# Kernel tuning notes

Hardware: AMD Instinct MI355X
Metric: run time of the kernel (lower is better)

Reference implementation:

```python
import jax, jax.numpy as jnp
import numpy as np

B, LQ, LIM = 4, 640, 1296
D_MODEL, NHEAD, DFF, MAX_DIST = 768, 12, 3072, 100
DK = D_MODEL // NHEAD
EPS = 1e-5


def _layer_norm(x, g, b):
    mu = jnp.mean(x, axis=-1, keepdims=True)
    var = jnp.mean(jnp.square(x - mu), axis=-1, keepdims=True)
    return (x - mu) * jax.lax.rsqrt(var + EPS) * g + b


def setup_inputs() -> dict:
    key = jax.random.key(0)
    ks = jax.random.split(key, 24)
    s = 0.02
    inp = {
        "docqa": jax.random.normal(ks[0], (B, LQ, D_MODEL), jnp.float32),
        "im_tokens": jax.random.normal(ks[1], (B, LIM, D_MODEL), jnp.float32),
        "docqa_x": jax.random.randint(ks[2], (B, LQ), 0, 1000, jnp.int32),
        "docqa_y": jax.random.randint(ks[3], (B, LQ), 0, 1000, jnp.int32),
        "im_tokens_x": jax.random.randint(ks[4], (B, LIM), 0, 1000, jnp.int32),
        "im_tokens_y": jax.random.randint(ks[5], (B, LIM), 0, 1000, jnp.int32),
        # attention projection params
        "Wq": jax.random.normal(ks[6], (D_MODEL, D_MODEL), jnp.float32) * s,
        "bq": jnp.zeros((D_MODEL,), jnp.float32),
        "Wk": jax.random.normal(ks[7], (D_MODEL, D_MODEL), jnp.float32) * s,
        "bk": jnp.zeros((D_MODEL,), jnp.float32),
        "Wv": jax.random.normal(ks[8], (D_MODEL, D_MODEL), jnp.float32) * s,
        "bv": jnp.zeros((D_MODEL,), jnp.float32),
        "Wo": jax.random.normal(ks[9], (D_MODEL, D_MODEL), jnp.float32) * s,
        "bo": jnp.zeros((D_MODEL,), jnp.float32),
        # relative position bias tables: (2*max_dist+1, nhead) per axis
        "bias_x": jax.random.normal(ks[10], (2 * MAX_DIST + 1, NHEAD), jnp.float32) * s,
        "bias_y": jax.random.normal(ks[11], (2 * MAX_DIST + 1, NHEAD), jnp.float32) * s,
        # FFN
        "W1": jax.random.normal(ks[12], (D_MODEL, DFF), jnp.float32) * s,
        "b1": jnp.zeros((DFF,), jnp.float32),
        "W2": jax.random.normal(ks[13], (DFF, D_MODEL), jnp.float32) * s,
        "b2": jnp.zeros((D_MODEL,), jnp.float32),
        # LayerNorms
        "g1": jnp.ones((D_MODEL,), jnp.float32),
        "be1": jnp.zeros((D_MODEL,), jnp.float32),
        "g2": jnp.ones((D_MODEL,), jnp.float32),
        "be2": jnp.zeros((D_MODEL,), jnp.float32),
    }
    return inp


def reference(docqa, im_tokens, docqa_x, docqa_y, im_tokens_x, im_tokens_y,
              Wq, bq, Wk, bk, Wv, bv, Wo, bo, bias_x, bias_y,
              W1, b1, W2, b2, g1, be1, g2, be2):
    # keys/values attend over concatenated image tokens + docqa tokens
    full = jnp.concatenate([im_tokens, docqa], axis=1)            # (B, Lk, D)
    full_x = jnp.concatenate([im_tokens_x, docqa_x], axis=1)      # (B, Lk)
    full_y = jnp.concatenate([im_tokens_y, docqa_y], axis=1)

    q = (docqa @ Wq + bq).reshape(B, LQ, NHEAD, DK)               # (B,Lq,H,Dk)
    k = (full @ Wk + bk).reshape(B, LQ + LIM, NHEAD, DK)
    v = (full @ Wv + bv).reshape(B, LQ + LIM, NHEAD, DK)

    scores = jnp.einsum("bqhd,bkhd->bhqk", q, k) / jnp.sqrt(jnp.float32(DK))

    # relative-position bias, clamped to [-max_dist, max_dist]
    rel_x = jnp.clip(docqa_x[:, :, None] - full_x[:, None, :], -MAX_DIST, MAX_DIST) + MAX_DIST
    rel_y = jnp.clip(docqa_y[:, :, None] - full_y[:, None, :], -MAX_DIST, MAX_DIST) + MAX_DIST
    pos_bias = bias_x[rel_x] + bias_y[rel_y]                      # (B,Lq,Lk,H)
    scores = scores + jnp.transpose(pos_bias, (0, 3, 1, 2))       # (B,H,Lq,Lk)

    attn = jax.nn.softmax(scores, axis=-1)
    ctx = jnp.einsum("bhqk,bkhd->bqhd", attn, v).reshape(B, LQ, D_MODEL)
    attn_out = ctx @ Wo + bo

    # residual + norm + FFN + residual + norm (dropout=0 in eval)
    src = _layer_norm(docqa + attn_out, g1, be1)
    ffn = jnp.maximum(src @ W1 + b1, 0.0) @ W2 + b2
    src = _layer_norm(src + ffn, g2, be2)
    return src
```

## Files before the change

### kernel.cpp

```cpp
#include <hip/hip_runtime.h>
#include <hip/hip_bf16.h>

constexpr int B      = 4;
constexpr int LQ     = 640;
constexpr int LIM    = 1296;
constexpr int LK     = LQ + LIM;
constexpr int DM     = 768;
constexpr int NHEAD  = 12;
constexpr int DK     = 64;
constexpr int DFF    = 3072;
constexpr int MAXD   = 100;
constexpr int M_DOC  = B * LQ;
constexpr int M_FULL = B * LK;
constexpr size_t ML_CNT = (size_t)B * NHEAD * LQ;
constexpr int NPREP  = M_FULL * (DM / 8) / 256;
constexpr int NSPLIT = 3;

typedef __attribute__((ext_vector_type(8))) short bf16x8_t;
typedef __attribute__((ext_vector_type(4))) float f32x4_t;

__device__ __forceinline__ float b2f(__hip_bfloat16 x) { return __bfloat162float(x); }

__device__ __forceinline__ float ldf(const void* p, size_t i, int f32flag) {
    return f32flag ? ((const float*)p)[i]
                   : b2f(((const __hip_bfloat16*)p)[i]);
}

__device__ __forceinline__ void gl_lds16(const void* g, void* l) {
    __builtin_amdgcn_global_load_lds(
        (const __attribute__((address_space(1))) unsigned int*)g,
        (__attribute__((address_space(3))) unsigned int*)l, 16, 0, 0);
}

__device__ __forceinline__ void wtrans_tile(const void* W, __hip_bfloat16* Wt,
                                            int f32, int K, int N, int n0, int k0,
                                            __hip_bfloat16 (*t)[33])
{
    const int tx = threadIdx.x & 31, ty = threadIdx.x >> 5;
#pragma unroll
    for (int j = 0; j < 4; ++j) {
        int k = ty + j * 8;
        t[k][tx] = __float2bfloat16(ldf(W, (size_t)(k0 + k) * N + n0 + tx, f32));
    }
    __syncthreads();
#pragma unroll
    for (int j = 0; j < 4; ++j) {
        int n = ty + j * 8;
        Wt[(size_t)(n0 + n) * K + k0 + tx] = t[tx][n];
    }
}

__global__ __launch_bounds__(256)
void prep_wt3_kernel(const void* __restrict__ g1, int* __restrict__ flagp,
                     const void* __restrict__ im, const void* __restrict__ docqa,
                     const int* __restrict__ dqx, const int* __restrict__ dqy,
                     const int* __restrict__ imx, const int* __restrict__ imy,
                     const void* __restrict__ Wq, const void* __restrict__ Wk,
                     const void* __restrict__ Wv,
                     __hip_bfloat16* __restrict__ fullA,
                     int* __restrict__ cxy,
                     __hip_bfloat16* __restrict__ Wt3)
{
    __shared__ __hip_bfloat16 t[32][33];
    const bool f32 = ((*(const unsigned*)g1) & 0xFFFFu) == 0u;
    const int bx = blockIdx.x;

    if (bx >= NPREP) {
        const int id  = bx - NPREP;
        const int wid = id / 576;
        const int tt  = id % 576;
        const void* W = (wid == 0) ? Wq : (wid == 1) ? Wk : Wv;
        wtrans_tile(W, Wt3 + (size_t)wid * DM * DM, f32 ? 1 : 0, DM, DM,
                    (tt % 24) * 32, (tt / 24) * 32, t);
        return;
    }

    if (bx == 0 && threadIdx.x == 0) *flagp = f32 ? 1 : 0;

    const int gid = bx * 256 + threadIdx.x;
    if (gid < B * LK) {
        int b = gid / LK, l = gid - b * LK;
        const int x = (l < LIM) ? imx[b * LIM + l] : dqx[b * LQ + l - LIM];
        const int y = (l < LIM) ? imy[b * LIM + l] : dqy[b * LQ + l - LIM];
        cxy[gid] = (x & 0xFFFF) | (y << 16);
    }

    const int row = gid / (DM / 8);
    const int col = (gid - row * (DM / 8)) * 8;
    const int b   = row / LK;
    const int l   = row - b * LK;
    const size_t srow = (l < LIM) ? ((size_t)(b * LIM + l)) * DM
                                  : ((size_t)(b * LQ + (l - LIM))) * DM;
    const void* src = (l < LIM) ? im : docqa;
    union { bf16x8_t v; __hip_bfloat16 h[8]; } pk;
    if (f32) {
        const float4* fp = (const float4*)((const float*)src + srow + col);
        float4 a = fp[0], c = fp[1];
        pk.h[0] = __float2bfloat16(a.x); pk.h[1] = __float2bfloat16(a.y);
        pk.h[2] = __float2bfloat16(a.z); pk.h[3] = __float2bfloat16(a.w);
        pk.h[4] = __float2bfloat16(c.x); pk.h[5] = __float2bfloat16(c.y);
        pk.h[6] = __float2bfloat16(c.z); pk.h[7] = __float2bfloat16(c.w);
    } else {
        pk.v = *(const bf16x8_t*)((const __hip_bfloat16*)src + srow + col);
    }
    *(bf16x8_t*)(fullA + (size_t)row * DM + col) = pk.v;
}

__global__ __launch_bounds__(256)
void qkv_gemm(const __hip_bfloat16* __restrict__ fullA,
              const __hip_bfloat16* __restrict__ Wt3,
              const void* __restrict__ bq,
              const void* __restrict__ bk,
              const void* __restrict__ bv,
              __hip_bfloat16* __restrict__ qout,
              __hip_bfloat16* __restrict__ kb,
              __hip_bfloat16* __restrict__ vtb,
              const int* __restrict__ flagp)
{
    __shared__ __hip_bfloat16 Als[128 * 32];
    __shared__ __hip_bfloat16 Bls[128 * 32];

    const int f32  = *flagp;
    const int tid  = threadIdx.x;
    const int lane = tid & 63;
    const int wave = tid >> 6;
    const int quad = lane >> 4;
    const int c16  = lane & 15;

    const int id = blockIdx.x;
    int n0, m0;
    if (id < 732) {
        n0 = DM + (id % 12) * 128;
        m0 = (id / 12) * 128;
    } else {
        const int t = id - 732;
        n0 = (t % 6) * 128;
        m0 = (t / 6) * 128;
    }
    const int seg = n0 / DM;

    const int wm   = (wave >> 1) * 64;
    const int wn   = (wave & 1) * 64;
    constexpr int K = DM;

    f32x4_t acc[4][4] = {};

    for (int k0 = 0; k0 < K; k0 += 32) {
#pragma unroll
        for (int p = 0; p < 2; ++p) {
            const int lin = p * 64 + lane;
            int row = wave * 32 + (lin >> 2);
            int gr  = m0 + row;
            if (seg == 0) {
                const int bb = gr / LQ;
                gr = bb * LK + LIM + (gr - bb * LQ);
            } else if (gr > M_FULL - 1) gr = M_FULL - 1;
            gl_lds16(fullA + (size_t)gr * K + k0 + (lin & 3) * 8,
                     Als + wave * 1024 + p * 512);
        }
#pragma unroll
        for (int p = 0; p < 2; ++p) {
            const int lin = p * 64 + lane;
            const int row = wave * 32 + (lin >> 2);
            gl_lds16(Wt3 + (size_t)(n0 + row) * K + k0 + (lin & 3) * 8,
                     Bls + wave * 1024 + p * 512);
        }
        __syncthreads();

        bf16x8_t af[4], bfr[4];
#pragma unroll
        for (int i = 0; i < 4; ++i)
            af[i] = *(const bf16x8_t*)(Als + (wm + i * 16 + c16) * 32 + quad * 8);
#pragma unroll
        for (int j = 0; j < 4; ++j)
            bfr[j] = *(const bf16x8_t*)(Bls + (wn + j * 16 + c16) * 32 + quad * 8);
#pragma unroll
        for (int i = 0; i < 4; ++i)
#pragma unroll
            for (int j = 0; j < 4; ++j)
                acc[i][j] = __builtin_amdgcn_mfma_f32_16x16x32_bf16(af[i], bfr[j], acc[i][j], 0, 0, 0);
        __syncthreads();
    }

    const void* bptr = (seg == 0) ? bq : (seg == 1) ? bk : bv;
#pragma unroll
    for (int j = 0; j < 4; ++j) {
        const int col  = n0 + wn + j * 16 + c16;
        const int ncol = col - seg * DM;
        const float bj = ldf(bptr, ncol, f32);
        if (seg == 2) {
            const int h = ncol >> 6, d = ncol & 63;
#pragma unroll
            for (int i = 0; i < 4; ++i) {
                const int rowb = m0 + wm + i * 16 + quad * 4;
                const int bb0  = rowb / LK;
                const int l0   = rowb - bb0 * LK;
                if (l0 + 3 < LK && rowb + 3 < M_FULL) {
                    union { ushort4 u4; __hip_bfloat16 hh[4]; } pk;
#pragma unroll
                    for (int r = 0; r < 4; ++r)
                        pk.hh[r] = __float2bfloat16(acc[i][j][r] + bj);
                    *(ushort4*)(vtb + ((size_t)((bb0 * NHEAD + h) * DK + d)) * LK + l0) = pk.u4;
                } else {
#pragma unroll
                    for (int r = 0; r < 4; ++r) {
                        const int row = rowb + r;
                        if (row < M_FULL) {
                            int bb = row / LK, l = row - bb * LK;
                            vtb[((size_t)((bb * NHEAD + h) * DK + d)) * LK + l] =
                                __float2bfloat16(acc[i][j][r] + bj);
                        }
                    }
                }
            }
        } else if (seg == 1) {
#pragma unroll
            for (int i = 0; i < 4; ++i) {
                const int rowb = m0 + wm + i * 16 + quad * 4;
#pragma unroll
                for (int r = 0; r < 4; ++r) {
                    const int row = rowb + r;
                    if (row < M_FULL)
                        kb[(size_t)row * DM + ncol] = __float2bfloat16(acc[i][j][r] + bj);
                }
            }
        } else {
#pragma unroll
            for (int i = 0; i < 4; ++i) {
                const int rowb = m0 + wm + i * 16 + quad * 4;
#pragma unroll
                for (int r = 0; r < 4; ++r)
                    qout[(size_t)(rowb + r) * DM + ncol] =
                        __float2bfloat16((acc[i][j][r] + bj) * 0.125f);
            }
        }
    }
}

__global__ __launch_bounds__(256)
void mfma_gemm_relu(const __hip_bfloat16* __restrict__ Abf,
                    const __hip_bfloat16* __restrict__ Wt,
                    const void* __restrict__ bias,
                    __hip_bfloat16* __restrict__ Cc,
                    const int* __restrict__ flagp,
                    int M, int N, int K)
{
    __shared__ __hip_bfloat16 Als[128 * 32];
    __shared__ __hip_bfloat16 Bls[128 * 32];

    const int f32  = *flagp;
    const int tid  = threadIdx.x;
    const int lane = tid & 63;
    const int wave = tid >> 6;
    const int quad = lane >> 4;
    const int c16  = lane & 15;
    const int n0   = blockIdx.x * 128;
    const int m0   = blockIdx.y * 128;
    const int wm   = (wave >> 1) * 64;
    const int wn   = (wave & 1) * 64;

    f32x4_t acc[4][4] = {};

    for (int k0 = 0; k0 < K; k0 += 32) {
#pragma unroll
        for (int p = 0; p < 2; ++p) {
            const int lin = p * 64 + lane;
            int row = wave * 32 + (lin >> 2);
            int gr  = m0 + row; if (gr > M - 1) gr = M - 1;
            gl_lds16(Abf + (size_t)gr * K + k0 + (lin & 3) * 8, Als + wave * 1024 + p * 512);
        }
#pragma unroll
        for (int p = 0; p < 2; ++p) {
            const int lin = p * 64 + lane;
            const int row = wave * 32 + (lin >> 2);
            gl_lds16(Wt + (size_t)(n0 + row) * K + k0 + (lin & 3) * 8,
                     Bls + wave * 1024 + p * 512);
        }
        __syncthreads();

        bf16x8_t af[4], bfr[4];
#pragma unroll
        for (int i = 0; i < 4; ++i)
            af[i] = *(const bf16x8_t*)(Als + (wm + i * 16 + c16) * 32 + quad * 8);
#pragma unroll
        for (int j = 0; j < 4; ++j)
            bfr[j] = *(const bf16x8_t*)(Bls + (wn + j * 16 + c16) * 32 + quad * 8);
#pragma unroll
        for (int i = 0; i < 4; ++i)
#pragma unroll
            for (int j = 0; j < 4; ++j)
                acc[i][j] = __builtin_amdgcn_mfma_f32_16x16x32_bf16(af[i], bfr[j], acc[i][j], 0, 0, 0);
        __syncthreads();
    }

#pragma unroll
    for (int j = 0; j < 4; ++j) {
        const int col = n0 + wn + j * 16 + c16;
        const float bj = ldf(bias, col, f32);
#pragma unroll
        for (int i = 0; i < 4; ++i) {
            const int rowb = m0 + wm + i * 16 + quad * 4;
#pragma unroll
            for (int r = 0; r < 4; ++r) {
                const int row = rowb + r;
                if (row < M) {
                    float v = fmaxf(acc[i][j][r] + bj, 0.f);
                    Cc[(size_t)row * N + col] = __float2bfloat16(v);
                }
            }
        }
    }
}

__global__ __launch_bounds__(256)
void sk_gemm(const __hip_bfloat16* __restrict__ Abf,
             const __hip_bfloat16* __restrict__ Wt,
             float* __restrict__ Cc,
             int M, int N, int K, int S)
{
    __shared__ __hip_bfloat16 Als[128 * 32];
    __shared__ __hip_bfloat16 Bls[128 * 32];

    const int tid  = threadIdx.x;
    const int lane = tid & 63;
    const int wave = tid >> 6;
    const int quad = lane >> 4;
    const int c16  = lane & 15;
    const int n0   = blockIdx.x * 128;
    const int m0   = blockIdx.y * 128;
    const int wm   = (wave >> 1) * 64;
    const int wn   = (wave & 1) * 64;
    const int kchunk = K / S;
    const int kbeg = blockIdx.z * kchunk;

    f32x4_t acc[4][4] = {};

    for (int k0 = kbeg; k0 < kbeg + kchunk; k0 += 32) {
#pragma unroll
        for (int p = 0; p < 2; ++p) {
            const int lin = p * 64 + lane;
            int row = wave * 32 + (lin >> 2);
            int gr  = m0 + row; if (gr > M - 1) gr = M - 1;
            gl_lds16(Abf + (size_t)gr * K + k0 + (lin & 3) * 8, Als + wave * 1024 + p * 512);
        }
#pragma unroll
        for (int p = 0; p < 2; ++p) {
            const int lin = p * 64 + lane;
            const int row = wave * 32 + (lin >> 2);
            gl_lds16(Wt + (size_t)(n0 + row) * K + k0 + (lin & 3) * 8,
                     Bls + wave * 1024 + p * 512);
        }
        __syncthreads();

        bf16x8_t af[4], bfr[4];
#pragma unroll
        for (int i = 0; i < 4; ++i)
            af[i] = *(const bf16x8_t*)(Als + (wm + i * 16 + c16) * 32 + quad * 8);
#pragma unroll
        for (int j = 0; j < 4; ++j)
            bfr[j] = *(const bf16x8_t*)(Bls + (wn + j * 16 + c16) * 32 + quad * 8);
#pragma unroll
        for (int i = 0; i < 4; ++i)
#pragma unroll
            for (int j = 0; j < 4; ++j)
                acc[i][j] = __builtin_amdgcn_mfma_f32_16x16x32_bf16(af[i], bfr[j], acc[i][j], 0, 0, 0);
        __syncthreads();
    }

#pragma unroll
    for (int j = 0; j < 4; ++j) {
        const int col = n0 + wn + j * 16 + c16;
#pragma unroll
        for (int i = 0; i < 4; ++i) {
            const int rowb = m0 + wm + i * 16 + quad * 4;
#pragma unroll
            for (int r = 0; r < 4; ++r) {
                const int row = rowb + r;
                if (row < M) atomicAdd(&Cc[(size_t)row * N + col], acc[i][j][r]);
            }
        }
    }
}

__global__ __launch_bounds__(256)
void attn_part_kernel(const __hip_bfloat16* __restrict__ Qb,
                      const __hip_bfloat16* __restrict__ Kb,
                      const __hip_bfloat16* __restrict__ Vtb,
                      const int* __restrict__ cxy,
                      const void* __restrict__ bias_x,
                      const void* __restrict__ bias_y,
                      __hip_bfloat16* __restrict__ pparts,
                      float* __restrict__ mlbase,
                      const int* __restrict__ flagp)
{
    constexpr int QT = 64, KT = 64;
    constexpr int QROW = 72;
    __shared__ char PQraw[QT * QROW * 2];
    __shared__ __hip_bfloat16 Ks[KT * DK];
    __shared__ __hip_bfloat16 Vs[DK * KT];
    __shared__ __hip_bfloat16 bxs[2 * MAXD + 1], bys[2 * MAXD + 1];
    __hip_bfloat16* Qs = (__hip_bfloat16*)PQraw;
    __hip_bfloat16* Ps = (__hip_bfloat16*)PQraw;

    const int f32  = *flagp;
    const int tid  = threadIdx.x;
    const int lane = tid & 63;
    const int wave = tid >> 6;
    const int quad = lane >> 4;
    const int c16  = lane & 15;

    const int id   = blockIdx.x;
    const int bh   = id % 48;
    const int rest = id / 48;
    const int s    = rest % NSPLIT;
    const int q0   = (rest / NSPLIT) * QT;
    const int b    = bh / NHEAD;
    const int h    = bh - b * NHEAD;
    const int kbeg = s * 640;
    const int kend = (s == NSPLIT - 1) ? LK : kbeg + 640;

    __hip_bfloat16* Op = pparts + (size_t)s * M_DOC * DM;
    float* mp = mlbase + (size_t)s * 2 * ML_CNT;
    float* lp = mp + ML_CNT;

    for (int i = tid; i < 2 * MAXD + 1; i += 256) {
        bxs[i] = __float2bfloat16(ldf(bias_x, (size_t)i * NHEAD + h, f32));
        bys[i] = __float2bfloat16(ldf(bias_y, (size_t)i * NHEAD + h, f32));
    }

    const __hip_bfloat16* kbase = Kb + ((size_t)(b * LK)) * DM + h * DK;
    const __hip_bfloat16* vbase = Vtb + ((size_t)((b * NHEAD + h) * DK)) * LK;
    const __hip_bfloat16* qbase = Qb + ((size_t)(b * LQ + q0)) * DM + h * DK;
    const int* cb_ = cxy + b * LK;

    {
        const int rsub0 = lane >> 3;
        const int cg0   = (lane & 7) ^ (rsub0 & 7);
#pragma unroll
        for (int p = 0; p < 2; ++p) {
            const int rl = wave * 16 + p * 8 + rsub0;
            gl_lds16(qbase + (size_t)rl * DM + cg0 * 8, Qs + (wave * 16 + p * 8) * DK);
        }
    }

    int qxp[4], qyp[4];
#pragma unroll
    for (int r = 0; r < 4; ++r) {
        const int v = cb_[LIM + q0 + wave * 16 + quad * 4 + r];
        qxp[r] = (v & 0xFFFF) + MAXD;
        qyp[r] = (v >> 16) + MAXD;
    }

    __syncthreads();

    const int sw  = c16 & 7;
    const int cA0 = (quad ^ sw) * 8;
    const int cA1 = ((quad + 4) ^ sw) * 8;
    const int rQ  = wave * 16 + c16;
    const bf16x8_t aq0 = *(const bf16x8_t*)(Qs + rQ * DK + cA0);
    const bf16x8_t aq1 = *(const bf16x8_t*)(Qs + rQ * DK + cA1);
    asm volatile("s_waitcnt lgkmcnt(0)" ::: "memory");
    __syncthreads();

    f32x4_t O[4] = {};
    float m_r[4], l_r[4];
#pragma unroll
    for (int r = 0; r < 4; ++r) { m_r[r] = -1e30f; l_r[r] = 0.f; }

    const int rsub = lane >> 3;
    const int cgl  = (lane & 7) ^ (rsub & 7);

    for (int k0 = kbeg; k0 < kend; k0 += KT) {
#pragma unroll
        for (int p = 0; p < 2; ++p) {
            const int rl = wave * 16 + p * 8 + rsub;
            int gr = k0 + rl; if (gr > LK - 1) gr = LK - 1;
            gl_lds16(kbase + (size_t)gr * DM + cgl * 8, Ks + (wave * 16 + p * 8) * DK);
        }
#pragma unroll
        for (int p = 0; p < 2; ++p) {
            const int dl = wave * 16 + p * 8 + rsub;
            int kks = k0 + cgl * 8; if (kks > LK - 8) kks = LK - 8;
            gl_lds16(vbase + (size_t)dl * LK + kks, Vs + (wave * 16 + p * 8) * KT);
        }
        __syncthreads();

        f32x4_t S[4];
#pragma unroll
        for (int jn = 0; jn < 4; ++jn) {
            const int rK = jn * 16 + c16;
            bf16x8_t bk0 = *(const bf16x8_t*)(Ks + rK * DK + cA0);
            bf16x8_t bk1 = *(const bf16x8_t*)(Ks + rK * DK + cA1);
            f32x4_t acc = {0.f, 0.f, 0.f, 0.f};
            acc = __builtin_amdgcn_mfma_f32_16x16x32_bf16(aq0, bk0, acc, 0, 0, 0);
            acc = __builtin_amdgcn_mfma_f32_16x16x32_bf16(aq1, bk1, acc, 0, 0, 0);
            S[jn] = acc;
        }
#pragma unroll
        for (int jn = 0; jn < 4; ++jn) {
            const int kg = k0 + jn * 16 + c16;
            const bool ok = kg < LK;
            const int kv = cb_[ok ? kg : LK - 1];
            const int kx = kv & 0xFFFF, ky = kv >> 16;
#pragma unroll
            for (int r = 0; r < 4; ++r) {
                int rx = min(max(qxp[r] - kx, 0), 2 * MAXD);
                int ry = min(max(qyp[r] - ky, 0), 2 * MAXD);
                float v = S[jn][r] + b2f(bxs[rx]) + b2f(bys[ry]);
                S[jn][r] = ok ? v : -1e30f;
            }
        }
        float alpha[4];
#pragma unroll
        for (int r = 0; r < 4; ++r) {
            float mx = fmaxf(fmaxf(S[0][r], S[1][r]), fmaxf(S[2][r], S[3][r]));
            mx = fmaxf(mx, __shfl_xor(mx, 1));
            mx = fmaxf(mx, __shfl_xor(mx, 2));
            mx = fmaxf(mx, __shfl_xor(mx, 4));
            mx = fmaxf(mx, __shfl_xor(mx, 8));
            const float mt = fmaxf(m_r[r], mx);
            const float al = __expf(m_r[r] - mt);
            float sum = 0.f;
#pragma unroll
            for (int jn = 0; jn < 4; ++jn) {
                float p = __expf(S[jn][r] - mt);
                S[jn][r] = p;
                sum += p;
            }
            m_r[r] = mt;
            l_r[r] = l_r[r] * al + sum;
            alpha[r] = al;
        }
#pragma unroll
        for (int jn = 0; jn < 4; ++jn)
#pragma unroll
            for (int r = 0; r < 4; ++r)
                Ps[(wave * 16 + quad * 4 + r) * QROW + jn * 16 + c16] = __float2bfloat16(S[jn][r]);
#pragma unroll
        for (int jd = 0; jd < 4; ++jd)
#pragma unroll
            for (int r = 0; r < 4; ++r) O[jd][r] *= alpha[r];
        bf16x8_t ap0 = *(const bf16x8_t*)(Ps + (wave * 16 + c16) * QROW + quad * 8);
        bf16x8_t ap1 = *(const bf16x8_t*)(Ps + (wave * 16 + c16) * QROW + 32 + quad * 8);
#pragma unroll
        for (int jd = 0; jd < 4; ++jd) {
            const int rV = jd * 16 + c16;
            bf16x8_t bv0 = *(const bf16x8_t*)(Vs + rV * KT + cA0);
            bf16x8_t bv1 = *(const bf16x8_t*)(Vs + rV * KT + cA1);
            O[jd] = __builtin_amdgcn_mfma_f32_16x16x32_bf16(ap0, bv0, O[jd], 0, 0, 0);
            O[jd] = __builtin_amdgcn_mfma_f32_16x16x32_bf16(ap1, bv1, O[jd], 0, 0, 0);
        }
        __syncthreads();
    }

#pragma unroll
    for (int r = 0; r < 4; ++r) {
        float ls = l_r[r];
        ls += __shfl_xor(ls, 1);
        ls += __shfl_xor(ls, 2);
        ls += __shfl_xor(ls, 4);
        ls += __shfl_xor(ls, 8);
        const int ql = wave * 16 + quad * 4 + r;
        const size_t grow = (size_t)(b * LQ + q0 + ql);
#pragma unroll
        for (int jd = 0; jd < 4; ++jd)
            Op[grow * DM + h * DK + jd * 16 + c16] = __float2bfloat16(O[jd][r]);
        if (c16 == 0) {
            size_t mli = ((size_t)b * NHEAD + h) * LQ + q0 + ql;
            mp[mli] = m_r[r];
            lp[mli] = ls;
        }
    }
}

__global__ __launch_bounds__(256)
void merge_wt_kernel(const __hip_bfloat16* __restrict__ pparts,
                     const float* __restrict__ mlbase,
                     __hip_bfloat16* __restrict__ ctx,
                     float* __restrict__ aof,
                     const void* __restrict__ Wo,
                     __hip_bfloat16* __restrict__ WtO,
                     const void* __restrict__ W1,
                     const void* __restrict__ W2,
                     __hip_bfloat16* __restrict__ W1t,
                     __hip_bfloat16* __restrict__ W2t,
                     const int* __restrict__ flagp)
{
    __shared__ __hip_bfloat16 t[32][33];
    const int bx = blockIdx.x;

    if (bx >= M_DOC + 576) {
        const int id = bx - (M_DOC + 576);
        const int f32 = *flagp;
        const bool second = id >= 2304;
        const void* W = second ? W2 : W1;
        __hip_bfloat16* dst = second ? W2t : W1t;
        const int K = second ? DFF : DM;
        const int N = second ? DM : DFF;
        const int tt = second ? id - 2304 : id;
        const int nt = N / 32;
        wtrans_tile(W, dst, f32, K, N, (tt % nt) * 32, (tt / nt) * 32, t);
        return;
    }
    if (bx >= M_DOC) {
        const int tt = bx - M_DOC;
        wtrans_tile(Wo, WtO, *flagp, DM, DM, (tt % 24) * 32, (tt / 24) * 32, t);
        return;
    }

    const int row = bx;
    const int b = row / LQ, q = row - b * LQ;
    const int tid = threadIdx.x;
#pragma unroll
    for (int i = 0; i < 3; ++i) {
        const int c = tid + i * 256;
        const int h = c >> 6;
        const size_t mli = ((size_t)b * NHEAD + h) * LQ + q;
        const float m0 = mlbase[mli],                  l0 = mlbase[ML_CNT + mli];
        const float m1 = mlbase[2 * ML_CNT + mli],     l1 = mlbase[3 * ML_CNT + mli];
        const float m2 = mlbase[4 * ML_CNT + mli],     l2 = mlbase[5 * ML_CNT + mli];
        const float mm = fmaxf(m0, fmaxf(m1, m2));
        const float w0 = __expf(m0 - mm), w1 = __expf(m1 - mm), w2 = __expf(m2 - mm);
        const float denom = l0 * w0 + l1 * w1 + l2 * w2;
        const size_t idx = (size_t)row * DM + c;
        const float v = (b2f(pparts[idx]) * w0 +
                         b2f(pparts[(size_t)M_DOC * DM + idx]) * w1 +
                         b2f(pparts[(size_t)2 * M_DOC * DM + idx]) * w2) / denom;
        ctx[idx] = __float2bfloat16(v);
        aof[idx] = 0.f;
    }
}

template<int MODE>
__global__ __launch_bounds__(256)
void ln_kernel(const void* __restrict__ Xin,
               const __hip_bfloat16* __restrict__ Xb,
               const float* __restrict__ Xf2f,
               const void* __restrict__ bias2,
               const void* __restrict__ g,
               const void* __restrict__ be,
               __hip_bfloat16* __restrict__ outb,
               void* __restrict__ outv,
               float* __restrict__ zbuf,
               const int* __restrict__ flagp)
{
    __shared__ float red1[4], red2[4];
    const int f32 = *flagp;
    const int row = blockIdx.x;
    const int tid = threadIdx.x;
    const int lane = tid & 63;
    const int wave = tid >> 6;

    float x[3];
#pragma unroll
    for (int i = 0; i < 3; ++i) {
        int c = tid + i * 256;
        size_t idx = (size_t)row * DM + c;
        float a  = (MODE == 0) ? ldf(Xin, idx, f32) : b2f(Xb[idx]);
        x[i] = a + Xf2f[idx] + ldf(bias2, c, f32);
    }
    float s1 = x[0] + x[1] + x[2];
    float s2 = x[0] * x[0] + x[1] * x[1] + x[2] * x[2];
#pragma unroll
    for (int off = 32; off > 0; off >>= 1) {
        s1 += __shfl_xor(s1, off);
        s2 += __shfl_xor(s2, off);
    }
    if (lane == 0) { red1[wave] = s1; red2[wave] = s2; }
    __syncthreads();
    s1 = red1[0] + red1[1] + red1[2] + red1[3];
    s2 = red2[0] + red2[1] + red2[2] + red2[3];
    float mu   = s1 * (1.f / DM);
    float var  = s2 * (1.f / DM) - mu * mu;
    float rstd = rsqrtf(var + 1e-5f);
#pragma unroll
    for (int i = 0; i < 3; ++i) {
        int c = tid + i * 256;
        size_t idx = (size_t)row * DM + c;
        float v = (x[i] - mu) * rstd * ldf(g, c, f32) + ldf(be, c, f32);
        if (MODE == 0) {
            outb[idx] = __float2bfloat16(v);
            zbuf[idx] = 0.f;
        } else {
            if (f32) ((float*)outv)[idx] = v;
            else     ((__hip_bfloat16*)outv)[idx] = __float2bfloat16(v);
        }
    }
}

extern "C" void kernel_launch(void* const* d_in, const int* in_sizes, int n_in,
                              void* d_out, int out_size, void* d_ws, size_t ws_size,
                              hipStream_t stream)
{
    const void* docqa = d_in[0];
    const void* im    = d_in[1];
    const int* dqx = (const int*)d_in[2];
    const int* dqy = (const int*)d_in[3];
    const int* imx = (const int*)d_in[4];
    const int* imy = (const int*)d_in[5];
    const void* Wq = d_in[6];
    const void* bq = d_in[7];
    const void* Wk = d_in[8];
    const void* bk = d_in[9];
    const void* Wv = d_in[10];
    const void* bv = d_in[11];
    const void* Wo = d_in[12];
    const void* bo = d_in[13];
    const void* bias_x = d_in[14];
    const void* bias_y = d_in[15];
    const void* W1 = d_in[16];
    const void* b1 = d_in[17];
    const void* W2 = d_in[18];
    const void* b2 = d_in[19];
    const void* g1  = d_in[20];
    const void* be1 = d_in[21];
    const void* g2  = d_in[22];
    const void* be2 = d_in[23];

    char* w = (char*)d_ws;
    int*            flagp = (int*)w;
    __hip_bfloat16* qR  = (__hip_bfloat16*)(w + 256);
    __hip_bfloat16* kb  = qR + (size_t)M_DOC  * DM;
    __hip_bfloat16* vtb = kb + (size_t)M_FULL * DM;
    __hip_bfloat16* cb  = vtb + (size_t)M_FULL * DM;
    char* cbB = (char*)cb;
    char* r1B = (char*)qR;

    __hip_bfloat16* fullA = cb;
    __hip_bfloat16* Wt3  = qR;
    int*            cxyp = (int*)(r1B + 3538944);
    __hip_bfloat16* WtO  = qR;
    __hip_bfloat16* qout = (__hip_bfloat16*)d_out;
    __hip_bfloat16* pparts = cb;
    float*          mlb  = (float*)(r1B + 1179648);
    __hip_bfloat16* ctx  = cb;
    __hip_bfloat16* src1 = cb;
    float*          fof  = (float*)(cbB + 3932160);
    float*          aof  = (float*)kb;
    __hip_bfloat16* W1t  = vtb;
    __hip_bfloat16* W2t  = vtb + (size_t)DFF * DM;
    __hip_bfloat16* mid  = qR;

    dim3 blk(256);

    prep_wt3_kernel<<<dim3(NPREP + 3 * 576), blk, 0, stream>>>(
        g1, flagp, im, docqa, dqx, dqy, imx, imy, Wq, Wk, Wv, fullA, cxyp, Wt3);
    qkv_gemm<<<dim3(732 + 120), blk, 0, stream>>>(
        fullA, Wt3, bq, bk, bv, qout, kb, vtb, flagp);
    attn_part_kernel<<<dim3(48 * 30), blk, 0, stream>>>(
        qout, kb, vtb, cxyp, bias_x, bias_y, pparts, mlb, flagp);
    merge_wt_kernel<<<dim3(M_DOC + 576 + 4608), blk, 0, stream>>>(
        pparts, mlb, ctx, aof, Wo, WtO, W1, W2, W1t, W2t, flagp);
    sk_gemm<<<dim3(DM / 128, M_DOC / 128, 4), blk, 0, stream>>>(
        ctx, WtO, aof, M_DOC, DM, DM, 4);
    ln_kernel<0><<<dim3(M_DOC), blk, 0, stream>>>(
        docqa, nullptr, aof, bo, g1, be1, src1, nullptr, fof, flagp);
    mfma_gemm_relu<<<dim3(DFF / 128, M_DOC / 128), blk, 0, stream>>>(
        src1, W1t, b1, mid, flagp, M_DOC, DFF, DM);
    sk_gemm<<<dim3(DM / 128, M_DOC / 128, 4), blk, 0, stream>>>(
        mid, W2t, fof, M_DOC, DM, DFF, 4);
    ln_kernel<1><<<dim3(M_DOC), blk, 0, stream>>>(
        nullptr, src1, fof, b2, g2, be2, nullptr, d_out, nullptr, flagp);
}
```

Measured before the change: 379.7 us.

## Double-buffer K/V tiles in attention kernel to overlap loads with compute

The attention partial kernel now keeps two LDS buffers each for K and V. It issues the global-to-LDS load for the next key tile before computing on the current one, and the per-iteration barrier that used to sit before the MFMAs is gone. The goal is to hide global load latency behind the QK and PV work. In exchange, LDS use per block roughly doubles for K/V, which can lower occupancy, and the last iteration issues one extra clamped prefetch that is never used.

New measurement: 378.1 us (median of 2 runs). No clear change (-0.4%).

```diff
diff --git a/kernel.cpp b/kernel.cpp
--- a/kernel.cpp
+++ b/kernel.cpp
@@ -396,8 +396,8 @@
     constexpr int QT = 64, KT = 64;
     constexpr int QROW = 72;
     __shared__ char PQraw[QT * QROW * 2];
-    __shared__ __hip_bfloat16 Ks[KT * DK];
-    __shared__ __hip_bfloat16 Vs[DK * KT];
+    __shared__ __hip_bfloat16 Ks[2 * KT * DK];
+    __shared__ __hip_bfloat16 Vs[2 * DK * KT];
     __shared__ __hip_bfloat16 bxs[2 * MAXD + 1], bys[2 * MAXD + 1];
     __hip_bfloat16* Qs = (__hip_bfloat16*)PQraw;
     __hip_bfloat16* Ps = (__hip_bfloat16*)PQraw;
@@ -433,14 +433,26 @@
     const __hip_bfloat16* qbase = Qb + ((size_t)(b * LQ + q0)) * DM + h * DK;
     const int* cb_ = cxy + b * LK;
 
-    {
-        const int rsub0 = lane >> 3;
-        const int cg0   = (lane & 7) ^ (rsub0 & 7);
-#pragma unroll
-        for (int p = 0; p < 2; ++p) {
-            const int rl = wave * 16 + p * 8 + rsub0;
-            gl_lds16(qbase + (size_t)rl * DM + cg0 * 8, Qs + (wave * 16 + p * 8) * DK);
-        }
+    const int rsub = lane >> 3;
+    const int cgl  = (lane & 7) ^ (rsub & 7);
+
+#pragma unroll
+    for (int p = 0; p < 2; ++p) {
+        const int rl = wave * 16 + p * 8 + rsub;
+        gl_lds16(qbase + (size_t)rl * DM + cgl * 8, Qs + (wave * 16 + p * 8) * DK);
+    }
+
+#pragma unroll
+    for (int p = 0; p < 2; ++p) {
+        const int rl = wave * 16 + p * 8 + rsub;
+        int gr = kbeg + rl; if (gr > LK - 1) gr = LK - 1;
+        gl_lds16(kbase + (size_t)gr * DM + cgl * 8, Ks + (wave * 16 + p * 8) * DK);
+    }
+#pragma unroll
+    for (int p = 0; p < 2; ++p) {
+        const int dl = wave * 16 + p * 8 + rsub;
+        int kks = kbeg + cgl * 8; if (kks > LK - 8) kks = LK - 8;
+        gl_lds16(vbase + (size_t)dl * LK + kks, Vs + (wave * 16 + p * 8) * KT);
     }
 
     int qxp[4], qyp[4];
@@ -467,30 +479,36 @@
 #pragma unroll
     for (int r = 0; r < 4; ++r) { m_r[r] = -1e30f; l_r[r] = 0.f; }
 
-    const int rsub = lane >> 3;
-    const int cgl  = (lane & 7) ^ (rsub & 7);
-
-    for (int k0 = kbeg; k0 < kend; k0 += KT) {
-#pragma unroll
-        for (int p = 0; p < 2; ++p) {
-            const int rl = wave * 16 + p * 8 + rsub;
-            int gr = k0 + rl; if (gr > LK - 1) gr = LK - 1;
-            gl_lds16(kbase + (size_t)gr * DM + cgl * 8, Ks + (wave * 16 + p * 8) * DK);
-        }
-#pragma unroll
-        for (int p = 0; p < 2; ++p) {
-            const int dl = wave * 16 + p * 8 + rsub;
-            int kks = k0 + cgl * 8; if (kks > LK - 8) kks = LK - 8;
-            gl_lds16(vbase + (size_t)dl * LK + kks, Vs + (wave * 16 + p * 8) * KT);
-        }
-        __syncthreads();
+    const int nt = (kend - kbeg + KT - 1) / KT;
+    int bi = 0;
+    for (int t = 0; t < nt; ++t) {
+        const int k0 = kbeg + t * KT;
+        {
+            const int kn = k0 + KT;
+            __hip_bfloat16* Kd = Ks + (bi ^ 1) * (KT * DK);
+            __hip_bfloat16* Vd = Vs + (bi ^ 1) * (KT * DK);
+#pragma unroll
+            for (int p = 0; p < 2; ++p) {
+                const int rl = wave * 16 + p * 8 + rsub;
+                int gr = kn + rl; if (gr > LK - 1) gr = LK - 1;
+                gl_lds16(kbase + (size_t)gr * DM + cgl * 8, Kd + (wave * 16 + p * 8) * DK);
+            }
+#pragma unroll
+            for (int p = 0; p < 2; ++p) {
+                const int dl = wave * 16 + p * 8 + rsub;
+                int kks = kn + cgl * 8; if (kks > LK - 8) kks = LK - 8;
+                gl_lds16(vbase + (size_t)dl * LK + kks, Vd + (wave * 16 + p * 8) * KT);
+            }
+        }
+        const __hip_bfloat16* Kc = Ks + bi * (KT * DK);
+        const __hip_bfloat16* Vc = Vs + bi * (KT * DK);
 
         f32x4_t S[4];
 #pragma unroll
         for (int jn = 0; jn < 4; ++jn) {
             const int rK = jn * 16 + c16;
-            bf16x8_t bk0 = *(const bf16x8_t*)(Ks + rK * DK + cA0);
-            bf16x8_t bk1 = *(const bf16x8_t*)(Ks + rK * DK + cA1);
+            bf16x8_t bk0 = *(const bf16x8_t*)(Kc + rK * DK + cA0);
+            bf16x8_t bk1 = *(const bf16x8_t*)(Kc + rK * DK + cA1);
             f32x4_t acc = {0.f, 0.f, 0.f, 0.f};
             acc = __builtin_amdgcn_mfma_f32_16x16x32_bf16(aq0, bk0, acc, 0, 0, 0);
             acc = __builtin_amdgcn_mfma_f32_16x16x32_bf16(aq1, bk1, acc, 0, 0, 0);
@@ -545,12 +563,13 @@
 #pragma unroll
         for (int jd = 0; jd < 4; ++jd) {
             const int rV = jd * 16 + c16;
-            bf16x8_t bv0 = *(const bf16x8_t*)(Vs + rV * KT + cA0);
-            bf16x8_t bv1 = *(const bf16x8_t*)(Vs + rV * KT + cA1);
+            bf16x8_t bv0 = *(const bf16x8_t*)(Vc + rV * KT + cA0);
+            bf16x8_t bv1 = *(const bf16x8_t*)(Vc + rV * KT + cA1);
             O[jd] = __builtin_amdgcn_mfma_f32_16x16x32_bf16(ap0, bv0, O[jd], 0, 0, 0);
             O[jd] = __builtin_amdgcn_mfma_f32_16x16x32_bf16(ap1, bv1, O[jd], 0, 0, 0);
         }
         __syncthreads();
+        bi ^= 1;
     }
 
 #pragma unroll
```
